# Kernel optimization log

Measured on AMD Instinct MI355X. Metric: run time of the kernel, lower is better.

Reference implementation:

```python
import jax, jax.numpy as jnp
import numpy as np

N = 100000; EI = 1600000; EC = 800000; G = 2000
FD = 512; H1 = 32; H2 = 32; EMB = 128; NH = 4
EPS = 1e-5


def setup_inputs() -> dict:
    key = jax.random.key(0)
    ks = jax.random.split(key, 30)
    p = lambda k, shp: (jax.random.normal(k, shp, jnp.float32) * 0.05)
    inp = {
        'feat': jax.random.normal(ks[0], (N, FD), jnp.float32),
        'inter_src': jax.random.randint(ks[1], (EI,), 0, N),
        'inter_dst': jax.random.randint(ks[2], (EI,), 0, N),
        'cross_src': jax.random.randint(ks[3], (EC,), 0, N),
        'cross_dst': jax.random.randint(ks[4], (EC,), 0, N),
        'graph_ids': jnp.sort(jax.random.randint(ks[5], (N,), 0, G)),
        # layer1
        'W_gc1': p(ks[6], (FD, NH * H1)), 'b_gc1': p(ks[7], (NH * H1,)),
        'W_gat1': p(ks[8], (FD, NH * H1)), 'al1': p(ks[9], (NH, H1)), 'ar1': p(ks[10], (NH, H1)), 'b_gat1': p(ks[11], (NH * H1,)),
        # layer2
        'W_gc2': p(ks[12], (NH * H1, NH * H2)), 'b_gc2': p(ks[13], (NH * H2,)),
        'W_gat2': p(ks[14], (NH * H1, NH * H2)), 'al2': p(ks[15], (NH, H2)), 'ar2': p(ks[16], (NH, H2)), 'b_gat2': p(ks[17], (NH * H2,)),
        # layer3
        'W_gc3': p(ks[18], (NH * H2, EMB)), 'b_gc3': p(ks[19], (EMB,)),
        'W_gat3': p(ks[20], (NH * H2, EMB)), 'al3': p(ks[21], (1, EMB)), 'ar3': p(ks[22], (1, EMB)), 'b_gat3': p(ks[23], (EMB,)),
        # batchnorms (gamma ones, beta zeros)
        'g1': jnp.ones((NH * H1,), jnp.float32), 'be1': jnp.zeros((NH * H1,), jnp.float32),
        'g2': jnp.ones((NH * H2,), jnp.float32), 'be2': jnp.zeros((NH * H2,), jnp.float32),
        'g3': jnp.ones((EMB,), jnp.float32), 'be3': jnp.zeros((EMB,), jnp.float32),
    }
    return inp


def _leaky(x):
    return jnp.where(x >= 0, x, 0.2 * x)


def _graph_conv(x, W, b, src, dst):
    # DGL GraphConv, norm='both': D_out^{-1/2} A D_in^{-1/2} X W + b (degrees clamped to >=1)
    ones = jnp.ones(src.shape[0], x.dtype)
    dout = jnp.clip(jax.ops.segment_sum(ones, src, num_segments=N), 1.0)
    din = jnp.clip(jax.ops.segment_sum(ones, dst, num_segments=N), 1.0)
    xw = (x @ W) * (dout ** -0.5)[:, None]          # project first (in >= out)
    agg = jax.ops.segment_sum(xw[src], dst, num_segments=N)
    return agg * (din ** -0.5)[:, None] + b


def _gat(x, W, al, ar, b, src, dst, H, d):
    # DGL GATConv: per-edge additive attention with edge softmax over incoming edges
    f = (x @ W).reshape(-1, H, d)                    # [N,H,d]
    el = jnp.sum(f * al, -1)                         # [N,H]
    er = jnp.sum(f * ar, -1)
    e = _leaky(el[src] + er[dst])                    # [E,H]
    m = jax.ops.segment_max(e, dst, num_segments=N)
    ex = jnp.exp(e - m[dst])
    s = jax.ops.segment_sum(ex, dst, num_segments=N)
    alpha = ex / s[dst]                              # [E,H]
    out = jax.ops.segment_sum(alpha[:, :, None] * f[src], dst, num_segments=N)
    return out + b.reshape(1, H, d), alpha


def _bn(x, g, b):
    mu = x.mean(0)
    v = jnp.mean((x - mu) ** 2, 0)
    return g * (x - mu) / jnp.sqrt(v + EPS) + b


def reference(feat, inter_src, inter_dst, cross_src, cross_dst, graph_ids,
              W_gc1, b_gc1, W_gat1, al1, ar1, b_gat1,
              W_gc2, b_gc2, W_gat2, al2, ar2, b_gat2,
              W_gc3, b_gc3, W_gat3, al3, ar3, b_gat3,
              g1, be1, g2, be2, g3, be3):
    h = feat
    hi = _graph_conv(h, W_gc1, b_gc1, inter_src, inter_dst)
    hc, _ = _gat(h, W_gat1, al1, ar1, b_gat1, cross_src, cross_dst, NH, H1)
    h = _bn(_leaky(hi + hc.reshape(N, -1)), g1, be1)
    hi = _graph_conv(h, W_gc2, b_gc2, inter_src, inter_dst)
    hc, _ = _gat(h, W_gat2, al2, ar2, b_gat2, cross_src, cross_dst, NH, H2)
    h = _bn(_leaky(hi + hc.reshape(N, -1)), g2, be2)
    h1 = _graph_conv(h, W_gc3, b_gc3, inter_src, inter_dst)
    h2, att = _gat(h, W_gat3, al3, ar3, b_gat3, cross_src, cross_dst, 1, EMB)
    h = _bn(h1 + h2[:, 0, :], g3, be3)
    att_sum = jax.ops.segment_sum(att[:, 0], cross_src, num_segments=N)   # [N]
    wh = h * att_sum[:, None]
    gsum = jax.ops.segment_sum(wh, graph_ids, num_segments=G)
    cnt = jnp.clip(jax.ops.segment_sum(jnp.ones(N, h.dtype), graph_ids, num_segments=G), 1.0)
    frag_embeddings = gsum / cnt[:, None]                                  # [G,EMB]
    return frag_embeddings, att_sum
```

## Files before the change

### kernel.cpp

```cpp
#include <hip/hip_runtime.h>
#include <math.h>

#define NN 100000
#define EIE 1600000
#define ECE 800000
#define GG 2000
#define FDIM 512
#define CC 128
#define BNEPS 1e-5f
#define SLOTI 48
#define SLOTC 32

static inline int cdiv(long a, long b){ return (int)((a+b-1)/b); }

typedef __attribute__((ext_vector_type(8))) short short8;
typedef __attribute__((ext_vector_type(4))) float f32x4;

__device__ __forceinline__ unsigned short f2bf(float f){
  unsigned u = __float_as_uint(f);
  u += 0x7fffu + ((u >> 16) & 1u);
  return (unsigned short)(u >> 16);
}
__device__ __forceinline__ float bf2f(unsigned short h){
  return __uint_as_float(((unsigned)h) << 16);
}
__device__ __forceinline__ float2 ldbf2(const unsigned short* p){
  ushort2 u = *(const ushort2*)p;
  return make_float2(bf2f(u.x), bf2f(u.y));
}

__global__ void k_fill_direct(const int* __restrict__ isrc, const int* __restrict__ idst,
                              const int* __restrict__ csrc, const int* __restrict__ cdst,
                              int* __restrict__ cnt_i, int* __restrict__ eid_i,
                              int* __restrict__ cnt_c, int* __restrict__ eid_c,
                              int* __restrict__ dout, float* __restrict__ att) {
  int e = blockIdx.x*256 + threadIdx.x;
  if (e < EIE) {
    int d = idst[e];
    int p = atomicAdd(&cnt_i[d], 1);
    if (p < SLOTI) eid_i[d*SLOTI + p] = isrc[e];
    atomicAdd(&dout[isrc[e]], 1);
  }
  if (e < ECE) {
    int d = cdst[e];
    int p = atomicAdd(&cnt_c[d], 1);
    if (p < SLOTC) eid_c[d*SLOTC + p] = csrc[e];
  }
  if (e < NN) att[e] = 0.f;
}

__device__ __forceinline__ size_t wt_off(int n, int k) {
  return (size_t)(k >> 5)*8192 + (((n >> 4)*4 + ((k >> 3) & 3))*16 + (n & 15))*8 + (k & 7);
}
__global__ void k_pack_all(const float* __restrict__ Wgc1, const float* __restrict__ Wgat1,
                           const float* __restrict__ Wgc2, const float* __restrict__ Wgat2,
                           const float* __restrict__ Wgc3, const float* __restrict__ Wgat3,
                           unsigned short* __restrict__ Wth1, unsigned short* __restrict__ Wtl1,
                           unsigned short* __restrict__ Wth2, unsigned short* __restrict__ Wtl2,
                           unsigned short* __restrict__ Wth3, unsigned short* __restrict__ Wtl3) {
  int t = blockIdx.x*256 + threadIdx.x;
  const float *W1, *W2; unsigned short *oh, *ol; int FIN, tt;
  if (t < 131072)      { W1=Wgc1; W2=Wgat1; oh=Wth1; ol=Wtl1; FIN=512; tt=t; }
  else if (t < 163840) { W1=Wgc2; W2=Wgat2; oh=Wth2; ol=Wtl2; FIN=128; tt=t-131072; }
  else if (t < 196608) { W1=Wgc3; W2=Wgat3; oh=Wth3; ol=Wtl3; FIN=128; tt=t-163840; }
  else return;
  int n = tt / FIN, k = tt % FIN;
  float v = (n < 128) ? W1[(size_t)k*128 + n] : W2[(size_t)k*128 + (n-128)];
  unsigned short h = f2bf(v);
  size_t o = wt_off(n, k);
  oh[o] = h;
  ol[o] = f2bf(v - bf2f(h));
}

template<int FIN, bool BF16IN, bool BN>
__global__ __launch_bounds__(512)
void k_gemm2(const float* __restrict__ xf, const unsigned short* __restrict__ xb,
             const unsigned short* __restrict__ Bh, const unsigned short* __restrict__ Bl,
             const int* __restrict__ rowdeg,
             const float* __restrict__ bnsc, const float* __restrict__ bnsh,
             unsigned short* __restrict__ Y1, unsigned short* __restrict__ Y2) {
  __shared__ __attribute__((aligned(16))) unsigned short sAh[4096];
  __shared__ __attribute__((aligned(16))) unsigned short sBh[8192];
  __shared__ __attribute__((aligned(16))) unsigned short sBl[8192];
  int tid = threadIdx.x;
  int row0 = blockIdx.x*128;
  int lane = tid & 63, wid = tid >> 6;
  int wm = wid >> 2, wn = wid & 3;
  int l15 = lane & 15, quad = lane >> 4;

  f32x4 acc[4][4];
  #pragma unroll
  for (int mt = 0; mt < 4; ++mt)
    #pragma unroll
    for (int nt = 0; nt < 4; ++nt) acc[mt][nt] = (f32x4){0.f,0.f,0.f,0.f};

  for (int k0 = 0; k0 < FIN; k0 += 32) {
    if (BF16IN) {
      int r = tid >> 2, c16 = tid & 3;
      int gr = row0 + r; if (gr > NN-1) gr = NN-1;
      short8 u = *(const short8*)(xb + (size_t)gr*CC + k0 + c16*8);
      short8 o;
      #pragma unroll
      for (int j = 0; j < 8; ++j) {
        float f = bf2f((unsigned short)u[j]);
        if (BN) f = f*bnsc[k0 + c16*8 + j] + bnsh[k0 + c16*8 + j];
        o[j] = (short)f2bf(f);
      }
      *(short8*)&sAh[(((r>>4)*4 + c16)*16 + (r&15))*8] = o;
    } else {
      #pragma unroll
      for (int i = 0; i < 2; ++i) {
        int idx = tid + i*512;
        int r = idx >> 3, c = idx & 7;
        int gr = row0 + r; if (gr > NN-1) gr = NN-1;
        float4 v = *(const float4*)(xf + (size_t)gr*FIN + k0 + c*4);
        ushort4 hh;
        hh.x = f2bf(v.x); hh.y = f2bf(v.y); hh.z = f2bf(v.z); hh.w = f2bf(v.w);
        *(ushort4*)&sAh[(((r>>4)*4 + (c>>1))*16 + (r&15))*8 + (c&1)*4] = hh;
      }
    }
    const unsigned short* bhk = Bh + (size_t)k0*256;
    const unsigned short* blk = Bl + (size_t)k0*256;
    #pragma unroll
    for (int i = 0; i < 2; ++i) {
      int idx = tid + i*512;
      *(float4*)&sBh[idx*8] = *(const float4*)(bhk + idx*8);
      *(float4*)&sBl[idx*8] = *(const float4*)(blk + idx*8);
    }
    __syncthreads();
    short8 ah[4];
    #pragma unroll
    for (int mt = 0; mt < 4; ++mt)
      ah[mt] = *(const short8*)&sAh[(((wm*4+mt)*4 + quad)*16 + l15)*8];
    #pragma unroll
    for (int nt = 0; nt < 4; ++nt) {
      int off = (((wn*4+nt)*4 + quad)*16 + l15)*8;
      short8 bh = *(const short8*)&sBh[off];
      short8 bl = *(const short8*)&sBl[off];
      #pragma unroll
      for (int mt = 0; mt < 4; ++mt) {
        acc[mt][nt] = __builtin_amdgcn_mfma_f32_16x16x32_bf16(ah[mt], bh, acc[mt][nt], 0,0,0);
        acc[mt][nt] = __builtin_amdgcn_mfma_f32_16x16x32_bf16(ah[mt], bl, acc[mt][nt], 0,0,0);
      }
    }
    __syncthreads();
  }
  unsigned short* Y = (wn < 2) ? Y1 : Y2;
  int colbase = (wn & 1)*64;
  #pragma unroll
  for (int mt = 0; mt < 4; ++mt) {
    #pragma unroll
    for (int r = 0; r < 4; ++r) {
      int row = row0 + (wm*4+mt)*16 + quad*4 + r;
      if (row >= NN) continue;
      float sc = (wn < 2) ? rsqrtf((float)max(rowdeg[row], 1)) : 1.0f;
      #pragma unroll
      for (int nt = 0; nt < 4; ++nt)
        Y[(size_t)row*CC + colbase + nt*16 + l15] = f2bf(acc[mt][nt][r]*sc);
    }
  }
}

template<int H>
__global__ __launch_bounds__(256)
void k_elr2(const unsigned short* __restrict__ f, const float* __restrict__ al,
            const float* __restrict__ ar, float* __restrict__ el, float* __restrict__ er,
            float* __restrict__ csq) {
  if (blockIdx.x == 0) csq[threadIdx.x] = 0.f;
  int lane = threadIdx.x & 63;
  int n = blockIdx.x*4 + (threadIdx.x >> 6);
  if (n >= NN) return;
  int c2 = lane*2;
  float2 v = ldbf2(f + (size_t)n*CC + c2);
  float2 a = *(const float2*)(al + c2);
  float2 b = *(const float2*)(ar + c2);
  float pa = v.x*a.x + v.y*a.y;
  float pb = v.x*b.x + v.y*b.y;
  const int W = (H == 1) ? 64 : 16;
  #pragma unroll
  for (int m = W>>1; m >= 1; m >>= 1) { pa += __shfl_xor(pa, m); pb += __shfl_xor(pb, m); }
  if ((lane & (W-1)) == 0) {
    int h = lane / W;
    el[(size_t)n*H + h] = pa;
    er[(size_t)n*H + h] = pb;
  }
}

template<int H, bool ATT, bool LEAKY>
__global__ __launch_bounds__(256)
void k_gather_fused(const unsigned short* __restrict__ A1, const unsigned short* __restrict__ A2,
                    const int* __restrict__ cnt_i, const int* __restrict__ eid_i,
                    const int* __restrict__ cnt_c, const int* __restrict__ eid_c,
                    const float* __restrict__ el, const float* __restrict__ er,
                    const float* __restrict__ bgc, const float* __restrict__ bgat,
                    unsigned short* __restrict__ out, float* __restrict__ att) {
  int lane = threadIdx.x & 63;
  int row = blockIdx.x*4 + (threadIdx.x >> 6);
  if (row >= NN) return;
  int grp = lane >> 4;
  int l4  = lane & 15;
  int c8  = l4*8;

  int deg = cnt_i[row];
  int lo = row*SLOTI, hi = lo + min(deg, SLOTI);
  float ax[8];
  #pragma unroll
  for (int k = 0; k < 8; ++k) ax[k] = 0.f;
  int j = lo + grp;
  for (; j + 4 < hi; j += 8) {
    int s0 = eid_i[j], s1 = eid_i[j+4];
    short8 u0 = *(const short8*)(A1 + (size_t)s0*CC + c8);
    short8 u1 = *(const short8*)(A1 + (size_t)s1*CC + c8);
    #pragma unroll
    for (int k = 0; k < 8; ++k)
      ax[k] += bf2f((unsigned short)u0[k]) + bf2f((unsigned short)u1[k]);
  }
  if (j < hi) {
    int s0 = eid_i[j];
    short8 u0 = *(const short8*)(A1 + (size_t)s0*CC + c8);
    #pragma unroll
    for (int k = 0; k < 8; ++k) ax[k] += bf2f((unsigned short)u0[k]);
  }
  float sc = rsqrtf((float)max(deg, 1));

  int h = (H == 1) ? 0 : (l4 >> 2);
  float erd = er[(size_t)row*H + h];
  int degc = cnt_c[row];
  int lo2 = row*SLOTC, hi2 = lo2 + min(degc, SLOTC);
  float gacc[8];
  #pragma unroll
  for (int k = 0; k < 8; ++k) gacc[k] = 0.f;
  float denom = 0.f;
  for (j = lo2 + grp; j < hi2; j += 4) {
    int s = eid_c[j];
    float v = el[(size_t)s*H + h] + erd;
    v = (v >= 0.f) ? v : 0.2f*v;
    float w = __expf(v);
    denom += w;
    short8 u = *(const short8*)(A2 + (size_t)s*CC + c8);
    #pragma unroll
    for (int k = 0; k < 8; ++k) gacc[k] += w * bf2f((unsigned short)u[k]);
  }

  #pragma unroll
  for (int m = 16; m <= 32; m <<= 1) {
    denom += __shfl_xor(denom, m);
    #pragma unroll
    for (int k = 0; k < 8; ++k) {
      ax[k]   += __shfl_xor(ax[k], m);
      gacc[k] += __shfl_xor(gacc[k], m);
    }
  }
  float inv = (denom > 0.f) ? 1.0f/denom : 0.f;

  if (ATT) {
    for (j = lo2 + grp; j < hi2; j += 4) {
      int s = eid_c[j];
      if (l4 == 0) {
        float v = el[(size_t)s*H] + erd;
        v = (v >= 0.f) ? v : 0.2f*v;
        atomicAdd(&att[s], __expf(v)*inv);
      }
    }
  }

  if (grp == 0) {
    float4 b1a = *(const float4*)(bgc + c8);
    float4 b1b = *(const float4*)(bgc + c8 + 4);
    float4 b2a = *(const float4*)(bgat + c8);
    float4 b2b = *(const float4*)(bgat + c8 + 4);
    float bb1[8] = {b1a.x,b1a.y,b1a.z,b1a.w,b1b.x,b1b.y,b1b.z,b1b.w};
    float bb2[8] = {b2a.x,b2a.y,b2a.z,b2a.w,b2b.x,b2b.y,b2b.z,b2b.w};
    short8 ov;
    #pragma unroll
    for (int k = 0; k < 8; ++k) {
      float o = ax[k]*sc + bb1[k] + gacc[k]*inv + bb2[k];
      if (LEAKY) o = (o >= 0.f) ? o : 0.2f*o;
      ov[k] = (short)f2bf(o);
    }
    *(short8*)(out + (size_t)row*CC + c8) = ov;
  }
}

__global__ __launch_bounds__(256)
void k_bn_stats(const unsigned short* __restrict__ t, float* __restrict__ csq) {
  __shared__ float red[4][128];
  int lane = threadIdx.x & 63, g = threadIdx.x >> 6;
  int c2 = lane*2;
  float s0=0.f, s1=0.f, q0=0.f, q1=0.f;
  for (int r = blockIdx.x*4 + g; r < NN; r += gridDim.x*4) {
    float2 v = ldbf2(t + (size_t)r*CC + c2);
    s0 += v.x; s1 += v.y; q0 += v.x*v.x; q1 += v.y*v.y;
  }
  red[g][c2] = s0; red[g][c2+1] = s1;
  __syncthreads();
  if (threadIdx.x < 128) {
    float a = red[0][threadIdx.x] + red[1][threadIdx.x] + red[2][threadIdx.x] + red[3][threadIdx.x];
    atomicAdd(&csq[threadIdx.x], a);
  }
  __syncthreads();
  red[g][c2] = q0; red[g][c2+1] = q1;
  __syncthreads();
  if (threadIdx.x < 128) {
    float a = red[0][threadIdx.x] + red[1][threadIdx.x] + red[2][threadIdx.x] + red[3][threadIdx.x];
    atomicAdd(&csq[128 + threadIdx.x], a);
  }
}

__global__ void k_bn_coef(const float* __restrict__ csq,
                          const float* __restrict__ g, const float* __restrict__ be,
                          float* __restrict__ sc, float* __restrict__ sh) {
  int c = threadIdx.x;
  float mu = csq[c] * (1.f/NN);
  float var = csq[128+c] * (1.f/NN) - mu*mu;
  float r = rsqrtf(var + BNEPS);
  float s = g[c]*r;
  sc[c] = s;
  sh[c] = be[c] - s*mu;
}

__global__ void k_pool_bn(const unsigned short* __restrict__ t, const float* __restrict__ att,
                          const int* __restrict__ gids, const float* __restrict__ bnsc,
                          const float* __restrict__ bnsh, float* __restrict__ frag) {
  int g = blockIdx.x;
  __shared__ int se[2];
  if (threadIdx.x < 2) {
    int target = g + threadIdx.x;
    int lo = 0, hi = NN;
    while (lo < hi) { int mid = (lo + hi) >> 1; if (gids[mid] < target) lo = mid + 1; else hi = mid; }
    se[threadIdx.x] = lo;
  }
  __syncthreads();
  int lo = se[0], hi = se[1];
  int col = threadIdx.x;
  float scv = bnsc[col], shv = bnsh[col];
  float acc = 0.f;
  for (int n = lo; n < hi; ++n) acc += (bf2f(t[(size_t)n*CC + col])*scv + shv) * att[n];
  frag[(size_t)g*CC + col] = acc / (float)max(hi - lo, 1);
}

template<int FIN, int H, bool BF16IN, bool BN, bool ATT, bool LEAKY>
static void run_layer(const float* xf, const unsigned short* xb, const float* bgc,
                      const float* al, const float* ar, const float* bgat,
                      const float* g, const float* be,
                      const int* cnt_i, const int* eid_i, const int* cnt_c, const int* eid_c,
                      const int* dout, const unsigned short* Wth, const unsigned short* Wtl,
                      unsigned short* A1, unsigned short* A2, unsigned short* B,
                      float* el, float* er, float* csq, float* bnsc, float* bnsh,
                      float* att, hipStream_t stream) {
  k_gemm2<FIN,BF16IN,BN><<<cdiv(NN,128), 512, 0, stream>>>(xf, xb, Wth, Wtl, dout, bnsc, bnsh, A1, A2);
  k_elr2<H><<<cdiv(NN,4), 256, 0, stream>>>(A2, al, ar, el, er, csq);
  k_gather_fused<H,ATT,LEAKY><<<cdiv(NN,4), 256, 0, stream>>>(A1, A2, cnt_i, eid_i,
                                                              cnt_c, eid_c, el, er,
                                                              bgc, bgat, B, att);
  k_bn_stats<<<256, 256, 0, stream>>>(B, csq);
  k_bn_coef<<<1, 128, 0, stream>>>(csq, g, be, bnsc, bnsh);
}

extern "C" void kernel_launch(void* const* d_in, const int* in_sizes, int n_in,
                              void* d_out, int out_size, void* d_ws, size_t ws_size,
                              hipStream_t stream) {
  const float* feat  = (const float*)d_in[0];
  const int* isrc    = (const int*)d_in[1];
  const int* idst    = (const int*)d_in[2];
  const int* csrc    = (const int*)d_in[3];
  const int* cdst    = (const int*)d_in[4];
  const int* gids    = (const int*)d_in[5];
  const float* W_gc1 = (const float*)d_in[6];  const float* b_gc1 = (const float*)d_in[7];
  const float* W_gat1= (const float*)d_in[8];  const float* al1   = (const float*)d_in[9];
  const float* ar1   = (const float*)d_in[10]; const float* b_gat1= (const float*)d_in[11];
  const float* W_gc2 = (const float*)d_in[12]; const float* b_gc2 = (const float*)d_in[13];
  const float* W_gat2= (const float*)d_in[14]; const float* al2   = (const float*)d_in[15];
  const float* ar2   = (const float*)d_in[16]; const float* b_gat2= (const float*)d_in[17];
  const float* W_gc3 = (const float*)d_in[18]; const float* b_gc3 = (const float*)d_in[19];
  const float* W_gat3= (const float*)d_in[20]; const float* al3   = (const float*)d_in[21];
  const float* ar3   = (const float*)d_in[22]; const float* b_gat3= (const float*)d_in[23];
  const float* g1 = (const float*)d_in[24]; const float* be1 = (const float*)d_in[25];
  const float* g2 = (const float*)d_in[26]; const float* be2 = (const float*)d_in[27];
  const float* g3 = (const float*)d_in[28]; const float* be3 = (const float*)d_in[29];

  const size_t NC = (size_t)NN*CC;
  float* el   = (float*)d_ws;
  float* er   = el + (size_t)NN*4;
  float* csq  = er + (size_t)NN*4;
  float* bnsc = csq + 256;
  float* bnsh = bnsc + CC;
  unsigned short* B  = (unsigned short*)(bnsh + CC);
  unsigned short* A1 = B + NC;
  unsigned short* A2 = A1 + NC;
  unsigned short* Wth1 = A2 + NC;
  unsigned short* Wtl1 = Wth1 + 256*FDIM;
  unsigned short* Wth2 = Wtl1 + 256*FDIM;
  unsigned short* Wtl2 = Wth2 + 256*CC;
  unsigned short* Wth3 = Wtl2 + 256*CC;
  unsigned short* Wtl3 = Wth3 + 256*CC;
  int* cnt_i  = (int*)(Wtl3 + 256*CC);
  int* cnt_c  = cnt_i + NN;
  int* dout   = cnt_c + NN;
  int* eid_i  = dout + NN;
  int* eid_c  = eid_i + (size_t)NN*SLOTI;

  float* frag = (float*)d_out;
  float* att  = frag + (size_t)GG*CC;

  hipMemsetAsync(cnt_i, 0, 3*(size_t)NN*sizeof(int), stream);
  k_fill_direct<<<cdiv(EIE,256), 256, 0, stream>>>(isrc, idst, csrc, cdst,
                                                   cnt_i, eid_i, cnt_c, eid_c, dout, att);
  k_pack_all<<<cdiv(196608,256), 256, 0, stream>>>(W_gc1, W_gat1, W_gc2, W_gat2, W_gc3, W_gat3,
                                                   Wth1, Wtl1, Wth2, Wtl2, Wth3, Wtl3);

  run_layer<FDIM,4,false,false,false,true>(feat, nullptr, b_gc1, al1, ar1, b_gat1, g1, be1,
                                           cnt_i, eid_i, cnt_c, eid_c, dout, Wth1, Wtl1,
                                           A1, A2, B, el, er, csq, bnsc, bnsh, nullptr, stream);
  run_layer<CC,4,true,true,false,true>(nullptr, B, b_gc2, al2, ar2, b_gat2, g2, be2,
                                       cnt_i, eid_i, cnt_c, eid_c, dout, Wth2, Wtl2,
                                       A1, A2, B, el, er, csq, bnsc, bnsh, nullptr, stream);
  run_layer<CC,1,true,true,true,false>(nullptr, B, b_gc3, al3, ar3, b_gat3, g3, be3,
                                       cnt_i, eid_i, cnt_c, eid_c, dout, Wth3, Wtl3,
                                       A1, A2, B, el, er, csq, bnsc, bnsh, att, stream);

  k_pool_bn<<<GG, 128, 0, stream>>>(B, att, gids, bnsc, bnsh, frag);
}
```

Baseline: 1.167 ms.

## Fuse edge-bucket fill with layer-1 GEMM and move degree scaling into gather

Adjacency-bucket filling and the first projection GEMM now run in one launch, with blocks interleaved (every fifth block does GEMM, the rest fill edges). The atomic-heavy fill and the compute-bound GEMM can then overlap on the GPU. Because the GEMM no longer waits for out-degrees, the D_out^{-1/2} scaling moves from the GEMM epilogue into the gather, adding a per-edge dout load and rsqrt. The larger launch with mixed block roles can hurt occupancy, and the gather does extra per-edge work.

```diff
diff --git a/kernel.cpp b/kernel.cpp
--- a/kernel.cpp
+++ b/kernel.cpp
@@ -10,6 +10,9 @@
 #define BNEPS 1e-5f
 #define SLOTI 48
 #define SLOTC 32
+#define GEMM1_BLOCKS 782
+#define FILL_BLOCKS 3128
+#define FUSED_BLOCKS 3910
 
 static inline int cdiv(long a, long b){ return (int)((a+b-1)/b); }
 
@@ -27,26 +30,6 @@
 __device__ __forceinline__ float2 ldbf2(const unsigned short* p){
   ushort2 u = *(const ushort2*)p;
   return make_float2(bf2f(u.x), bf2f(u.y));
-}
-
-__global__ void k_fill_direct(const int* __restrict__ isrc, const int* __restrict__ idst,
-                              const int* __restrict__ csrc, const int* __restrict__ cdst,
-                              int* __restrict__ cnt_i, int* __restrict__ eid_i,
-                              int* __restrict__ cnt_c, int* __restrict__ eid_c,
-                              int* __restrict__ dout, float* __restrict__ att) {
-  int e = blockIdx.x*256 + threadIdx.x;
-  if (e < EIE) {
-    int d = idst[e];
-    int p = atomicAdd(&cnt_i[d], 1);
-    if (p < SLOTI) eid_i[d*SLOTI + p] = isrc[e];
-    atomicAdd(&dout[isrc[e]], 1);
-  }
-  if (e < ECE) {
-    int d = cdst[e];
-    int p = atomicAdd(&cnt_c[d], 1);
-    if (p < SLOTC) eid_c[d*SLOTC + p] = csrc[e];
-  }
-  if (e < NN) att[e] = 0.f;
 }
 
 __device__ __forceinline__ size_t wt_off(int n, int k) {
@@ -72,11 +55,105 @@
   ol[o] = f2bf(v - bf2f(h));
 }
 
-template<int FIN, bool BF16IN, bool BN>
 __global__ __launch_bounds__(512)
-void k_gemm2(const float* __restrict__ xf, const unsigned short* __restrict__ xb,
+void k_fill_gemm1(const int* __restrict__ isrc, const int* __restrict__ idst,
+                  const int* __restrict__ csrc, const int* __restrict__ cdst,
+                  int* __restrict__ cnt_i, int* __restrict__ eid_i,
+                  int* __restrict__ cnt_c, int* __restrict__ eid_c,
+                  int* __restrict__ dout, float* __restrict__ att,
+                  const float* __restrict__ xf,
+                  const unsigned short* __restrict__ Bh, const unsigned short* __restrict__ Bl,
+                  unsigned short* __restrict__ Y1, unsigned short* __restrict__ Y2) {
+  __shared__ __attribute__((aligned(16))) unsigned short sAh[4096];
+  __shared__ __attribute__((aligned(16))) unsigned short sBh[8192];
+  __shared__ __attribute__((aligned(16))) unsigned short sBl[8192];
+  int r = blockIdx.x;
+  int tid = threadIdx.x;
+
+  if (r % 5 != 0) {
+    int fi = r - 1 - (r-1)/5;
+    int e = fi*512 + tid;
+    if (e < EIE) {
+      int d = idst[e];
+      int p = atomicAdd(&cnt_i[d], 1);
+      if (p < SLOTI) eid_i[d*SLOTI + p] = isrc[e];
+      atomicAdd(&dout[isrc[e]], 1);
+    }
+    if (e < ECE) {
+      int d = cdst[e];
+      int p = atomicAdd(&cnt_c[d], 1);
+      if (p < SLOTC) eid_c[d*SLOTC + p] = csrc[e];
+    }
+    if (e < NN) att[e] = 0.f;
+    return;
+  }
+
+  int row0 = (r/5)*128;
+  int lane = tid & 63, wid = tid >> 6;
+  int wm = wid >> 2, wn = wid & 3;
+  int l15 = lane & 15, quad = lane >> 4;
+
+  f32x4 acc[4][4];
+  #pragma unroll
+  for (int mt = 0; mt < 4; ++mt)
+    #pragma unroll
+    for (int nt = 0; nt < 4; ++nt) acc[mt][nt] = (f32x4){0.f,0.f,0.f,0.f};
+
+  for (int k0 = 0; k0 < FDIM; k0 += 32) {
+    #pragma unroll
+    for (int i = 0; i < 2; ++i) {
+      int idx = tid + i*512;
+      int rr = idx >> 3, c = idx & 7;
+      int gr = row0 + rr; if (gr > NN-1) gr = NN-1;
+      float4 v = *(const float4*)(xf + (size_t)gr*FDIM + k0 + c*4);
+      ushort4 hh;
+      hh.x = f2bf(v.x); hh.y = f2bf(v.y); hh.z = f2bf(v.z); hh.w = f2bf(v.w);
+      *(ushort4*)&sAh[(((rr>>4)*4 + (c>>1))*16 + (rr&15))*8 + (c&1)*4] = hh;
+    }
+    const unsigned short* bhk = Bh + (size_t)k0*256;
+    const unsigned short* blk = Bl + (size_t)k0*256;
+    #pragma unroll
+    for (int i = 0; i < 2; ++i) {
+      int idx = tid + i*512;
+      *(float4*)&sBh[idx*8] = *(const float4*)(bhk + idx*8);
+      *(float4*)&sBl[idx*8] = *(const float4*)(blk + idx*8);
+    }
+    __syncthreads();
+    short8 ah[4];
+    #pragma unroll
+    for (int mt = 0; mt < 4; ++mt)
+      ah[mt] = *(const short8*)&sAh[(((wm*4+mt)*4 + quad)*16 + l15)*8];
+    #pragma unroll
+    for (int nt = 0; nt < 4; ++nt) {
+      int off = (((wn*4+nt)*4 + quad)*16 + l15)*8;
+      short8 bh = *(const short8*)&sBh[off];
+      short8 bl = *(const short8*)&sBl[off];
+      #pragma unroll
+      for (int mt = 0; mt < 4; ++mt) {
+        acc[mt][nt] = __builtin_amdgcn_mfma_f32_16x16x32_bf16(ah[mt], bh, acc[mt][nt], 0,0,0);
+        acc[mt][nt] = __builtin_amdgcn_mfma_f32_16x16x32_bf16(ah[mt], bl, acc[mt][nt], 0,0,0);
+      }
+    }
+    __syncthreads();
+  }
+  unsigned short* Y = (wn < 2) ? Y1 : Y2;
+  int colbase = (wn & 1)*64;
+  #pragma unroll
+  for (int mt = 0; mt < 4; ++mt) {
+    #pragma unroll
+    for (int rr = 0; rr < 4; ++rr) {
+      int row = row0 + (wm*4+mt)*16 + quad*4 + rr;
+      if (row >= NN) continue;
+      #pragma unroll
+      for (int nt = 0; nt < 4; ++nt)
+        Y[(size_t)row*CC + colbase + nt*16 + l15] = f2bf(acc[mt][nt][rr]);
+    }
+  }
+}
+
+__global__ __launch_bounds__(512)
+void k_gemm2(const unsigned short* __restrict__ xb,
              const unsigned short* __restrict__ Bh, const unsigned short* __restrict__ Bl,
-             const int* __restrict__ rowdeg,
              const float* __restrict__ bnsc, const float* __restrict__ bnsh,
              unsigned short* __restrict__ Y1, unsigned short* __restrict__ Y2) {
   __shared__ __attribute__((aligned(16))) unsigned short sAh[4096];
@@ -94,31 +171,19 @@
     #pragma unroll
     for (int nt = 0; nt < 4; ++nt) acc[mt][nt] = (f32x4){0.f,0.f,0.f,0.f};
 
-  for (int k0 = 0; k0 < FIN; k0 += 32) {
-    if (BF16IN) {
-      int r = tid >> 2, c16 = tid & 3;
-      int gr = row0 + r; if (gr > NN-1) gr = NN-1;
-      short8 u = *(const short8*)(xb + (size_t)gr*CC + k0 + c16*8);
-      short8 o;
-      #pragma unroll
-      for (int j = 0; j < 8; ++j) {
-        float f = bf2f((unsigned short)u[j]);
-        if (BN) f = f*bnsc[k0 + c16*8 + j] + bnsh[k0 + c16*8 + j];
-        o[j] = (short)f2bf(f);
-      }
-      *(short8*)&sAh[(((r>>4)*4 + c16)*16 + (r&15))*8] = o;
-    } else {
-      #pragma unroll
-      for (int i = 0; i < 2; ++i) {
-        int idx = tid + i*512;
-        int r = idx >> 3, c = idx & 7;
-        int gr = row0 + r; if (gr > NN-1) gr = NN-1;
-        float4 v = *(const float4*)(xf + (size_t)gr*FIN + k0 + c*4);
-        ushort4 hh;
-        hh.x = f2bf(v.x); hh.y = f2bf(v.y); hh.z = f2bf(v.z); hh.w = f2bf(v.w);
-        *(ushort4*)&sAh[(((r>>4)*4 + (c>>1))*16 + (r&15))*8 + (c&1)*4] = hh;
-      }
-    }
+  for (int k0 = 0; k0 < CC; k0 += 32) {
+    int rr = tid >> 2, c16 = tid & 3;
+    int gr = row0 + rr; if (gr > NN-1) gr = NN-1;
+    short8 u = *(const short8*)(xb + (size_t)gr*CC + k0 + c16*8);
+    short8 o;
+    #pragma unroll
+    for (int j = 0; j < 8; ++j) {
+      float f = bf2f((unsigned short)u[j]);
+      f = f*bnsc[k0 + c16*8 + j] + bnsh[k0 + c16*8 + j];
+      o[j] = (short)f2bf(f);
+    }
+    *(short8*)&sAh[(((rr>>4)*4 + c16)*16 + (rr&15))*8] = o;
+
     const unsigned short* bhk = Bh + (size_t)k0*256;
     const unsigned short* blk = Bl + (size_t)k0*256;
     #pragma unroll
@@ -150,13 +215,12 @@
   #pragma unroll
   for (int mt = 0; mt < 4; ++mt) {
     #pragma unroll
-    for (int r = 0; r < 4; ++r) {
-      int row = row0 + (wm*4+mt)*16 + quad*4 + r;
+    for (int rr = 0; rr < 4; ++rr) {
+      int row = row0 + (wm*4+mt)*16 + quad*4 + rr;
       if (row >= NN) continue;
-      float sc = (wn < 2) ? rsqrtf((float)max(rowdeg[row], 1)) : 1.0f;
       #pragma unroll
       for (int nt = 0; nt < 4; ++nt)
-        Y[(size_t)row*CC + colbase + nt*16 + l15] = f2bf(acc[mt][nt][r]*sc);
+        Y[(size_t)row*CC + colbase + nt*16 + l15] = f2bf(acc[mt][nt][rr]);
     }
   }
 }
@@ -191,6 +255,7 @@
 void k_gather_fused(const unsigned short* __restrict__ A1, const unsigned short* __restrict__ A2,
                     const int* __restrict__ cnt_i, const int* __restrict__ eid_i,
                     const int* __restrict__ cnt_c, const int* __restrict__ eid_c,
+                    const int* __restrict__ dout,
                     const float* __restrict__ el, const float* __restrict__ er,
                     const float* __restrict__ bgc, const float* __restrict__ bgat,
                     unsigned short* __restrict__ out, float* __restrict__ att) {
@@ -209,17 +274,20 @@
   int j = lo + grp;
   for (; j + 4 < hi; j += 8) {
     int s0 = eid_i[j], s1 = eid_i[j+4];
+    float d0 = rsqrtf((float)max(dout[s0], 1));
+    float d1 = rsqrtf((float)max(dout[s1], 1));
     short8 u0 = *(const short8*)(A1 + (size_t)s0*CC + c8);
     short8 u1 = *(const short8*)(A1 + (size_t)s1*CC + c8);
     #pragma unroll
     for (int k = 0; k < 8; ++k)
-      ax[k] += bf2f((unsigned short)u0[k]) + bf2f((unsigned short)u1[k]);
+      ax[k] += d0*bf2f((unsigned short)u0[k]) + d1*bf2f((unsigned short)u1[k]);
   }
   if (j < hi) {
     int s0 = eid_i[j];
+    float d0 = rsqrtf((float)max(dout[s0], 1));
     short8 u0 = *(const short8*)(A1 + (size_t)s0*CC + c8);
     #pragma unroll
-    for (int k = 0; k < 8; ++k) ax[k] += bf2f((unsigned short)u0[k]);
+    for (int k = 0; k < 8; ++k) ax[k] += d0*bf2f((unsigned short)u0[k]);
   }
   float sc = rsqrtf((float)max(deg, 1));
 
@@ -337,24 +405,6 @@
   float acc = 0.f;
   for (int n = lo; n < hi; ++n) acc += (bf2f(t[(size_t)n*CC + col])*scv + shv) * att[n];
   frag[(size_t)g*CC + col] = acc / (float)max(hi - lo, 1);
-}
-
-template<int FIN, int H, bool BF16IN, bool BN, bool ATT, bool LEAKY>
-static void run_layer(const float* xf, const unsigned short* xb, const float* bgc,
-                      const float* al, const float* ar, const float* bgat,
-                      const float* g, const float* be,
-                      const int* cnt_i, const int* eid_i, const int* cnt_c, const int* eid_c,
-                      const int* dout, const unsigned short* Wth, const unsigned short* Wtl,
-                      unsigned short* A1, unsigned short* A2, unsigned short* B,
-                      float* el, float* er, float* csq, float* bnsc, float* bnsh,
-                      float* att, hipStream_t stream) {
-  k_gemm2<FIN,BF16IN,BN><<<cdiv(NN,128), 512, 0, stream>>>(xf, xb, Wth, Wtl, dout, bnsc, bnsh, A1, A2);
-  k_elr2<H><<<cdiv(NN,4), 256, 0, stream>>>(A2, al, ar, el, er, csq);
-  k_gather_fused<H,ATT,LEAKY><<<cdiv(NN,4), 256, 0, stream>>>(A1, A2, cnt_i, eid_i,
-                                                              cnt_c, eid_c, el, er,
-                                                              bgc, bgat, B, att);
-  k_bn_stats<<<256, 256, 0, stream>>>(B, csq);
-  k_bn_coef<<<1, 128, 0, stream>>>(csq, g, be, bnsc, bnsh);
 }
 
 extern "C" void kernel_launch(void* const* d_in, const int* in_sizes, int n_in,
@@ -404,20 +454,34 @@
   float* att  = frag + (size_t)GG*CC;
 
   hipMemsetAsync(cnt_i, 0, 3*(size_t)NN*sizeof(int), stream);
-  k_fill_direct<<<cdiv(EIE,256), 256, 0, stream>>>(isrc, idst, csrc, cdst,
-                                                   cnt_i, eid_i, cnt_c, eid_c, dout, att);
   k_pack_all<<<cdiv(196608,256), 256, 0, stream>>>(W_gc1, W_gat1, W_gc2, W_gat2, W_gc3, W_gat3,
                                                    Wth1, Wtl1, Wth2, Wtl2, Wth3, Wtl3);
-
-  run_layer<FDIM,4,false,false,false,true>(feat, nullptr, b_gc1, al1, ar1, b_gat1, g1, be1,
-                                           cnt_i, eid_i, cnt_c, eid_c, dout, Wth1, Wtl1,
-                                           A1, A2, B, el, er, csq, bnsc, bnsh, nullptr, stream);
-  run_layer<CC,4,true,true,false,true>(nullptr, B, b_gc2, al2, ar2, b_gat2, g2, be2,
-                                       cnt_i, eid_i, cnt_c, eid_c, dout, Wth2, Wtl2,
-                                       A1, A2, B, el, er, csq, bnsc, bnsh, nullptr, stream);
-  run_layer<CC,1,true,true,true,false>(nullptr, B, b_gc3, al3, ar3, b_gat3, g3, be3,
-                                       cnt_i, eid_i, cnt_c, eid_c, dout, Wth3, Wtl3,
-                                       A1, A2, B, el, er, csq, bnsc, bnsh, att, stream);
+  k_fill_gemm1<<<FUSED_BLOCKS, 512, 0, stream>>>(isrc, idst, csrc, cdst,
+                                                 cnt_i, eid_i, cnt_c, eid_c, dout, att,
+                                                 feat, Wth1, Wtl1, A1, A2);
+
+  k_elr2<4><<<cdiv(NN,4), 256, 0, stream>>>(A2, al1, ar1, el, er, csq);
+  k_gather_fused<4,false,true><<<cdiv(NN,4), 256, 0, stream>>>(A1, A2, cnt_i, eid_i,
+                                                               cnt_c, eid_c, dout, el, er,
+                                                               b_gc1, b_gat1, B, nullptr);
+  k_bn_stats<<<256, 256, 0, stream>>>(B, csq);
+  k_bn_coef<<<1, 128, 0, stream>>>(csq, g1, be1, bnsc, bnsh);
+
+  k_gemm2<<<cdiv(NN,128), 512, 0, stream>>>(B, Wth2, Wtl2, bnsc, bnsh, A1, A2);
+  k_elr2<4><<<cdiv(NN,4), 256, 0, stream>>>(A2, al2, ar2, el, er, csq);
+  k_gather_fused<4,false,true><<<cdiv(NN,4), 256, 0, stream>>>(A1, A2, cnt_i, eid_i,
+                                                               cnt_c, eid_c, dout, el, er,
+                                                               b_gc2, b_gat2, B, nullptr);
+  k_bn_stats<<<256, 256, 0, stream>>>(B, csq);
+  k_bn_coef<<<1, 128, 0, stream>>>(csq, g2, be2, bnsc, bnsh);
+
+  k_gemm2<<<cdiv(NN,128), 512, 0, stream>>>(B, Wth3, Wtl3, bnsc, bnsh, A1, A2);
+  k_elr2<1><<<cdiv(NN,4), 256, 0, stream>>>(A2, al3, ar3, el, er, csq);
+  k_gather_fused<1,true,false><<<cdiv(NN,4), 256, 0, stream>>>(A1, A2, cnt_i, eid_i,
+                                                               cnt_c, eid_c, dout, el, er,
+                                                               b_gc3, b_gat3, B, att);
+  k_bn_stats<<<256, 256, 0, stream>>>(B, csq);
+  k_bn_coef<<<1, 128, 0, stream>>>(csq, g3, be3, bnsc, bnsh);
 
   k_pool_bn<<<GG, 128, 0, stream>>>(B, att, gids, bnsc, bnsh, frag);
 }
```

Result: faster. 1.037 ms (-11.2%).
